# Performance work log

Measured on AMD Instinct MI355X. Metric: run time of the kernel, lower is better.

The kernel has to match this reference:

```python
import jax, jax.numpy as jnp
import numpy as np

B, N, D, H = 8, 2048, 1024, 1024

def setup_inputs() -> dict:
    key = jax.random.key(0)
    ks = jax.random.split(key, 7)
    s = 1.0 / np.sqrt(D)
    return {
        "x": jax.random.normal(ks[0], (B, N, D), dtype=jnp.float32),
        "Wq": jax.random.uniform(ks[1], (D, H), jnp.float32, -s, s),
        "bq": jax.random.uniform(ks[2], (H,), jnp.float32, -s, s),
        "Wk": jax.random.uniform(ks[3], (D, H), jnp.float32, -s, s),
        "bk": jax.random.uniform(ks[4], (H,), jnp.float32, -s, s),
        "Wv": jax.random.uniform(ks[5], (D, H), jnp.float32, -s, s),
        "bv": jax.random.uniform(ks[6], (H,), jnp.float32, -s, s),
    }

def reference(x, Wq, bq, Wk, bk, Wv, bv):
    # q, k, v: [B, N, H]
    q = jnp.einsum('bnd,dh->bnh', x, Wq) + bq
    k = jnp.einsum('bnd,dh->bnh', x, Wk) + bk
    v = jnp.einsum('bnd,dh->bnh', x, Wv) + bv
    scale = 1.0 / jnp.sqrt(jnp.asarray(q.shape[-1], q.dtype))
    score = jnp.einsum('bqh,bkh->bqk', q, k) * scale  # [B, N, N]
    causal = jnp.tril(jnp.ones((q.shape[1], q.shape[1]), dtype=bool))
    score = jnp.where(causal, score, -jnp.inf)
    attn = jax.nn.softmax(score, axis=-1)
    # dropout p=0.0 -> identity (deterministic reference)
    return jnp.einsum('bqk,bkh->bqh', attn, v)
```

## Files before the change

### kernel.cpp

```cpp
#include <hip/hip_runtime.h>
#include <hip/hip_bf16.h>
#include <stdint.h>

#define BB 8
#define NN 2048
#define DD 1024
#define HH 1024

using f32x4 = __attribute__((ext_vector_type(4))) float;
using s16x8 = __attribute__((ext_vector_type(8))) short;

__device__ __forceinline__ short f2bf(float f){
  union { float f; uint32_t u; } v; v.f = f;
  uint32_t r = (v.u + 0x7fffu + ((v.u >> 16) & 1u)) >> 16;
  return (short)r;
}
__device__ __forceinline__ float bf2f(short s){
  union { uint32_t u; float f; } v; v.u = ((uint32_t)(uint16_t)s) << 16; return v.f;
}

#define MFMA(a,b,c) __builtin_amdgcn_mfma_f32_16x16x32_bf16((a),(b),(c),0,0,0)

#define GL16(gp, lp) __builtin_amdgcn_global_load_lds( \
    (const __attribute__((address_space(1))) void*)(gp), \
    (__attribute__((address_space(3))) void*)(lp), 16, 0, 0)

__global__ __launch_bounds__(256) void k_conv_x(const float* __restrict__ x,
                                                short* __restrict__ xb){
  int gid = blockIdx.x*256 + threadIdx.x;
  const float4* xv = (const float4*)x;
  float4 a = xv[(size_t)gid*2], b2 = xv[(size_t)gid*2+1];
  s16x8 o;
  o[0]=f2bf(a.x);  o[1]=f2bf(a.y);  o[2]=f2bf(a.z);  o[3]=f2bf(a.w);
  o[4]=f2bf(b2.x); o[5]=f2bf(b2.y); o[6]=f2bf(b2.z); o[7]=f2bf(b2.w);
  *(s16x8*)(xb + (size_t)gid*8) = o;
}

__global__ __launch_bounds__(256) void k_conv_w(const float* __restrict__ Wq,
                                                const float* __restrict__ Wk,
                                                const float* __restrict__ Wv,
                                                short* __restrict__ Wt){
  __shared__ float tile[64][65];
  int bx = blockIdx.x; int mat = bx >> 8; int ti = bx & 255;
  int d0 = (ti >> 4) << 6, h0 = (ti & 15) << 6;
  const float* W = (mat==0) ? Wq : (mat==1 ? Wk : Wv);
  int t = threadIdx.x;
  for (int i=0;i<16;i++){ int e = i*256 + t; int r = e>>6, c = e&63;
    tile[r][c] = W[(size_t)(d0+r)*HH + h0 + c]; }
  __syncthreads();
  for (int i=0;i<16;i++){ int e = i*256 + t; int r = e>>6, c = e&63;
    Wt[(size_t)(mat*HH + h0 + r)*DD + d0 + c] = f2bf(tile[c][r]); }
}

__global__ __launch_bounds__(512,2) void k_gemm(const short* __restrict__ Aw,
                                                const short* __restrict__ Bw,
                                                const float* __restrict__ bq,
                                                const float* __restrict__ bk,
                                                const float* __restrict__ bv,
                                                short* __restrict__ Qw,
                                                short* __restrict__ Kw,
                                                short* __restrict__ Vt){
  __shared__ short Al[4][256*32];
  __shared__ short Bl[4][256*32];
  const int t = threadIdx.x, l = t & 63, w = t >> 6;
  const int g = l >> 4, c = l & 15;
  const int bid = blockIdx.x;
  const int bm = (bid & 7)*8 + ((bid >> 3) & 7);
  const int bn = bid >> 6;
  const int m0 = bm << 8, c0 = bn << 8;
  const int wr = w >> 2, wc = w & 3;
  f32x4 acc[8][4] = {};

  const int sr = t >> 2, sch = t & 3;
  const int u0 = sch ^ ((sr >> 1) & 3);
  const int u1 = sch ^ (((sr + 128) >> 1) & 3);
  const short* A0 = Aw + (size_t)(m0 + sr)*DD + u0*8;
  const short* A1 = Aw + (size_t)(m0 + sr + 128)*DD + u1*8;
  const short* B0 = Bw + (size_t)(c0 + sr)*DD + u0*8;
  const short* B1 = Bw + (size_t)(c0 + sr + 128)*DD + u1*8;
  const int d0b = sr*64 + sch*16, d1b = (sr+128)*64 + sch*16;
  auto stage = [&](int kt){
    int s = kt & 3, ko = kt*32;
    GL16(A0 + ko, (char*)&Al[s][0] + d0b);
    GL16(A1 + ko, (char*)&Al[s][0] + d1b);
    GL16(B0 + ko, (char*)&Bl[s][0] + d0b);
    GL16(B1 + ko, (char*)&Bl[s][0] + d1b);
  };

  int aoff[8], boff[4];
  #pragma unroll
  for (int mi=0;mi<8;mi++){
    int row = wr*128 + mi*16 + c;
    aoff[mi] = row*32 + (g ^ ((row>>1)&3))*8;
  }
  #pragma unroll
  for (int ni=0;ni<4;ni++){
    int row = wc*64 + ni*16 + c;
    boff[ni] = row*32 + (g ^ ((row>>1)&3))*8;
  }

  auto body = [&](int kt, bool dostage){
    int s = kt & 3;
    __builtin_amdgcn_sched_barrier(0);
    __builtin_amdgcn_s_barrier();
    __builtin_amdgcn_sched_barrier(0);
    s16x8 bfr[4], af[8];
    #pragma unroll
    for (int ni=0;ni<4;ni++) bfr[ni] = *(const s16x8*)&Bl[s][boff[ni]];
    #pragma unroll
    for (int mi=0;mi<8;mi++) af[mi] = *(const s16x8*)&Al[s][aoff[mi]];
    if (dostage) stage(kt+3);
    __builtin_amdgcn_s_setprio(1);
    #pragma unroll
    for (int mi=0;mi<8;mi++)
      #pragma unroll
      for (int ni=0;ni<4;ni++)
        acc[mi][ni] = MFMA(bfr[ni], af[mi], acc[mi][ni]);
    __builtin_amdgcn_s_setprio(0);
  };

  stage(0); stage(1); stage(2);
  for (int kt = 0; kt < 30; ++kt){
    asm volatile("s_waitcnt vmcnt(8)" ::: "memory");
    body(kt, kt < 29);
  }
  asm volatile("s_waitcnt vmcnt(4)" ::: "memory");
  body(30, false);
  asm volatile("s_waitcnt vmcnt(0)" ::: "memory");
  body(31, false);

  const int mat = bn >> 2;
  const float* bias = (mat==0) ? bq : (mat==1 ? bk : bv);
  if (mat < 2){
    short* Outp = (mat==0) ? Qw : Kw;
    #pragma unroll
    for (int ni=0;ni<4;ni++){
      int col0 = (bn & 3)*256 + wc*64 + ni*16 + g*4;
      float4 bv4 = *(const float4*)&bias[col0];
      #pragma unroll
      for (int mi=0;mi<8;mi++){
        int orow = m0 + wr*128 + mi*16 + c;
        short4 pk;
        pk.x = f2bf(acc[mi][ni][0] + bv4.x);
        pk.y = f2bf(acc[mi][ni][1] + bv4.y);
        pk.z = f2bf(acc[mi][ni][2] + bv4.z);
        pk.w = f2bf(acc[mi][ni][3] + bv4.w);
        *(short4*)&Outp[(size_t)orow*HH + col0] = pk;
      }
    }
  } else {
    short* S = (w < 4) ? ((short*)&Al[0][0] + w*4352)
                       : ((short*)&Bl[0][0] + (w-4)*4352);
    const int bb = m0 >> 11;
    const int nbase = m0 & 2047;
    const int hglob0 = (bn & 3)*256 + wc*64;
    #pragma unroll
    for (int rr = 0; rr < 2; ++rr){
      const int R = 2*wr + rr;
      asm volatile("" ::: "memory");
      #pragma unroll
      for (int ni=0;ni<4;ni++){
        int col0 = hglob0 + ni*16 + g*4;
        float4 bv4 = *(const float4*)&bias[col0];
        #pragma unroll
        for (int mi2=0;mi2<4;mi2++){
          short4 pk;
          pk.x = f2bf(acc[rr*4+mi2][ni][0] + bv4.x);
          pk.y = f2bf(acc[rr*4+mi2][ni][1] + bv4.y);
          pk.z = f2bf(acc[rr*4+mi2][ni][2] + bv4.z);
          pk.w = f2bf(acc[rr*4+mi2][ni][3] + bv4.w);
          *(short4*)&S[(mi2*16 + c)*68 + ni*16 + g*4] = pk;
        }
      }
      asm volatile("" ::: "memory");
      #pragma unroll
      for (int k=0;k<8;++k){
        int hr = (l>>3) + k*8;
        int ng = l & 7;
        s16x8 sv;
        #pragma unroll
        for (int e=0;e<8;e++) sv[e] = S[(ng*8+e)*68 + hr];
        *(s16x8*)&Vt[((size_t)bb*HH + hglob0 + hr)*NN + nbase + R*64 + ng*8] = sv;
      }
    }
  }
}

__global__ __launch_bounds__(512) void k_s(const short* __restrict__ Qw,
                                           const short* __restrict__ Kw,
                                           short* __restrict__ Pp){
  __shared__ short Ql[128*32];
  __shared__ short Kl[256*32];
  const int t = threadIdx.x, l = t & 63, w = t >> 6;
  const int g = l >> 4, c = l & 15;
  int p = blockIdx.x; int b = p & 7; int si = p >> 3;
  int tr = 0; while ((((tr+2)*(tr+2)) >> 2) <= si) tr++;
  int tcp = si - (((tr+1)*(tr+1)) >> 2);
  const float SC_EXP = 0.04508422002783268f;
  const int wq = w >> 2, wk = w & 3;
  f32x4 acc[4][4] = {};

  const int sr = t >> 2, sch = t & 3;
  const int su  = sch ^ ((sr >> 1) & 3);
  const int su2 = sch ^ (((sr + 128) >> 1) & 3);
  const short* Qs  = Qw + ((size_t)(b*NN + tr*128  + sr))*HH + su*8;
  const short* Ks0 = Kw + ((size_t)(b*NN + tcp*256 + sr))*HH + su*8;
  const short* Ks1 = Kw + ((size_t)(b*NN + tcp*256 + sr + 128))*HH + su2*8;

  const int rchunk = (g ^ ((c>>1)&3)) * 8;
  int qoff[4], koff[4];
  #pragma unroll
  for (int mi=0;mi<4;mi++) qoff[mi] = (wq*64 + mi*16 + c)*32 + rchunk;
  #pragma unroll
  for (int ni=0;ni<4;ni++) koff[ni] = (wk*64 + ni*16 + c)*32 + rchunk;

  for (int kt = 0; kt < 32; ++kt){
    int ko = kt*32;
    __syncthreads();
    GL16(Qs  + ko, (char*)Ql + t*16);
    GL16(Ks0 + ko, (char*)Kl + t*16);
    GL16(Ks1 + ko, (char*)Kl + 8192 + t*16);
    __syncthreads();
    s16x8 qf[4], kf[4];
    #pragma unroll
    for (int ni=0;ni<4;ni++) kf[ni] = *(const s16x8*)&Kl[koff[ni]];
    #pragma unroll
    for (int mi=0;mi<4;mi++) qf[mi] = *(const s16x8*)&Ql[qoff[mi]];
    #pragma unroll
    for (int mi=0;mi<4;mi++)
      #pragma unroll
      for (int ni=0;ni<4;ni++)
        acc[mi][ni] = MFMA(kf[ni], qf[mi], acc[mi][ni]);
  }

  short* Pt = Pp + ((size_t)(b*72 + si))*32768;
  #pragma unroll
  for (int ni=0;ni<4;ni++){
    int pc0 = wk*64 + ni*16 + g*4;
    #pragma unroll
    for (int mi=0;mi<4;mi++){
      int pr = wq*64 + mi*16 + c;
      short4 pk;
      #pragma unroll
      for (int i=0;i<4;i++){
        bool keep = (tcp*256 + pc0 + i) <= (tr*128 + pr);
        float pv = keep ? exp2f(acc[mi][ni][i]*SC_EXP) : 0.f;
        ((short*)&pk)[i] = f2bf(pv);
      }
      *(short4*)&Pt[pr*256 + pc0] = pk;
    }
  }
}

__global__ __launch_bounds__(512) void k_pv(const short* __restrict__ Pp,
                                            const short* __restrict__ Vt,
                                            float* __restrict__ out){
  __shared__ short Pl[128*32];
  __shared__ short Vl[256*32];
  const int t = threadIdx.x, l = t & 63, w = t >> 6;
  const int g = l >> 4, c = l & 15;
  int p = blockIdx.x;
  int r = p >> 8, j = p & 255;
  int tr = r ? (15 - (j >> 4)) : (j >> 4);
  int id = r ? (16 + (j & 15)) : (j & 15);
  int b = id & 7, hc = id >> 3;
  const short* Pb = Pp + ((size_t)(b*72 + (((tr+1)*(tr+1))>>2)))*32768;
  const int wq = w >> 2, wh = w & 3;
  f32x4 acc[4][4] = {};
  float ls[4] = {0.f,0.f,0.f,0.f};

  const int sr = t >> 2, sch = t & 3;
  const int su  = sch ^ ((sr >> 1) & 3);
  const int su2 = sch ^ (((sr + 128) >> 1) & 3);
  const short* Vs0 = Vt + ((size_t)(b*HH + hc*256 + sr))*NN + su*8;
  const short* Vs1 = Vt + ((size_t)(b*HH + hc*256 + sr + 128))*NN + su2*8;

  const int rchunk = (g ^ ((c>>1)&3)) * 8;
  int poff[4], voff[4];
  #pragma unroll
  for (int mi=0;mi<4;mi++) poff[mi] = (wq*64 + mi*16 + c)*32 + rchunk;
  #pragma unroll
  for (int ni=0;ni<4;ni++) voff[ni] = (wh*64 + ni*16 + c)*32 + rchunk;

  const int nst = ((tr + 2) >> 1) * 8;
  for (int kt = 0; kt < nst; ++kt){
    const short* Ps = Pb + (size_t)(kt>>3)*32768 + (kt&7)*32;
    __syncthreads();
    GL16(Ps + sr*256 + su*8, (char*)Pl + t*16);
    GL16(Vs0 + kt*32, (char*)Vl + t*16);
    GL16(Vs1 + kt*32, (char*)Vl + 8192 + t*16);
    __syncthreads();
    s16x8 pf[4], vf[4];
    #pragma unroll
    for (int ni=0;ni<4;ni++) vf[ni] = *(const s16x8*)&Vl[voff[ni]];
    #pragma unroll
    for (int mi=0;mi<4;mi++) pf[mi] = *(const s16x8*)&Pl[poff[mi]];
    #pragma unroll
    for (int mi=0;mi<4;mi++){
      #pragma unroll
      for (int e=0;e<8;e++) ls[mi] += bf2f(pf[mi][e]);
    }
    #pragma unroll
    for (int mi=0;mi<4;mi++)
      #pragma unroll
      for (int ni=0;ni<4;ni++)
        acc[mi][ni] = MFMA(vf[ni], pf[mi], acc[mi][ni]);
  }
  #pragma unroll
  for (int mi=0;mi<4;mi++){
    ls[mi] += __shfl_xor(ls[mi], 16);
    ls[mi] += __shfl_xor(ls[mi], 32);
  }
  #pragma unroll
  for (int mi=0;mi<4;mi++){
    float linv = 1.0f / ls[mi];
    int orow = tr*128 + wq*64 + mi*16 + c;
    #pragma unroll
    for (int ni=0;ni<4;ni++){
      int h0 = hc*256 + wh*64 + ni*16 + g*4;
      float4 o4;
      o4.x = acc[mi][ni][0]*linv; o4.y = acc[mi][ni][1]*linv;
      o4.z = acc[mi][ni][2]*linv; o4.w = acc[mi][ni][3]*linv;
      *(float4*)&out[((size_t)(b*NN + orow))*HH + h0] = o4;
    }
  }
}

extern "C" void kernel_launch(void* const* d_in, const int* in_sizes, int n_in,
                              void* d_out, int out_size, void* d_ws, size_t ws_size,
                              hipStream_t stream) {
  const float* x  = (const float*)d_in[0];
  const float* Wq = (const float*)d_in[1];
  const float* bq = (const float*)d_in[2];
  const float* Wk = (const float*)d_in[3];
  const float* bk = (const float*)d_in[4];
  const float* Wv = (const float*)d_in[5];
  const float* bv = (const float*)d_in[6];
  char* ws = (char*)d_ws;
  short* xb = (short*)(ws);
  short* Pp = (short*)(ws);
  short* Wt = (short*)(ws + 33554432u);
  short* Qw = (short*)(ws + 41943040u);
  short* Kw = (short*)(ws + 75497472u);
  short* Vt = (short*)(ws + 109051904u);

  k_conv_x<<<8192, 256, 0, stream>>>(x, xb);
  k_conv_w<<<768, 256, 0, stream>>>(Wq, Wk, Wv, Wt);
  k_gemm<<<768, 512, 0, stream>>>(xb, Wt, bq, bk, bv, Qw, Kw, Vt);
  k_s<<<576, 512, 0, stream>>>(Qw, Kw, Pp);
  k_pv<<<512, 512, 0, stream>>>(Pp, Vt, (float*)d_out);
}
```

Measured before the change: 281.4 us.

## Load GEMM B operand directly to registers, drop B shared-memory staging

In the QKV projection GEMM, the B (weight) tiles no longer go through LDS. Each wave loads its B fragments straight from global memory into registers, double-buffered one k-step ahead, while A keeps its 4-stage LDS pipeline. This halves LDS usage, which could allow higher occupancy, and removes the LDS reads for B. The cost is redundant global loads of B across the two wave rows, more registers, and an extra sync plus an unpadded transpose scratch layout in the V epilogue that may cause bank conflicts.

New measurement: 330.7 us. +17.5%, slower.

```diff
diff --git a/kernel.cpp b/kernel.cpp
--- a/kernel.cpp
+++ b/kernel.cpp
@@ -61,7 +61,6 @@
                                                 short* __restrict__ Kw,
                                                 short* __restrict__ Vt){
   __shared__ short Al[4][256*32];
-  __shared__ short Bl[4][256*32];
   const int t = threadIdx.x, l = t & 63, w = t >> 6;
   const int g = l >> 4, c = l & 15;
   const int bid = blockIdx.x;
@@ -76,58 +75,61 @@
   const int u1 = sch ^ (((sr + 128) >> 1) & 3);
   const short* A0 = Aw + (size_t)(m0 + sr)*DD + u0*8;
   const short* A1 = Aw + (size_t)(m0 + sr + 128)*DD + u1*8;
-  const short* B0 = Bw + (size_t)(c0 + sr)*DD + u0*8;
-  const short* B1 = Bw + (size_t)(c0 + sr + 128)*DD + u1*8;
   const int d0b = sr*64 + sch*16, d1b = (sr+128)*64 + sch*16;
-  auto stage = [&](int kt){
+  auto stageA = [&](int kt){
     int s = kt & 3, ko = kt*32;
     GL16(A0 + ko, (char*)&Al[s][0] + d0b);
     GL16(A1 + ko, (char*)&Al[s][0] + d1b);
-    GL16(B0 + ko, (char*)&Bl[s][0] + d0b);
-    GL16(B1 + ko, (char*)&Bl[s][0] + d1b);
   };
 
-  int aoff[8], boff[4];
+  int aoff[8];
   #pragma unroll
   for (int mi=0;mi<8;mi++){
     int row = wr*128 + mi*16 + c;
     aoff[mi] = row*32 + (g ^ ((row>>1)&3))*8;
   }
-  #pragma unroll
-  for (int ni=0;ni<4;ni++){
-    int row = wc*64 + ni*16 + c;
-    boff[ni] = row*32 + (g ^ ((row>>1)&3))*8;
-  }
-
-  auto body = [&](int kt, bool dostage){
-    int s = kt & 3;
+  const short* Bp[4];
+  #pragma unroll
+  for (int ni=0;ni<4;ni++)
+    Bp[ni] = Bw + (size_t)(c0 + wc*64 + ni*16 + c)*DD + g*8;
+
+  s16x8 bfrE[4], bfrO[4];
+
+  auto body = [&](int kt, s16x8 (&cur)[4], s16x8 (&nxt)[4]){
+    if (kt == 0)      { asm volatile("s_waitcnt vmcnt(4)" ::: "memory"); }
+    else if (kt < 30) { asm volatile("s_waitcnt vmcnt(2)" ::: "memory"); }
+    else              { asm volatile("s_waitcnt vmcnt(0)" ::: "memory"); }
     __builtin_amdgcn_sched_barrier(0);
     __builtin_amdgcn_s_barrier();
     __builtin_amdgcn_sched_barrier(0);
-    s16x8 bfr[4], af[8];
-    #pragma unroll
-    for (int ni=0;ni<4;ni++) bfr[ni] = *(const s16x8*)&Bl[s][boff[ni]];
+    const int s = kt & 3;
+    s16x8 af[8];
     #pragma unroll
     for (int mi=0;mi<8;mi++) af[mi] = *(const s16x8*)&Al[s][aoff[mi]];
-    if (dostage) stage(kt+3);
+    if (kt < 31){
+      const int ko = (kt+1)*32;
+      #pragma unroll
+      for (int ni=0;ni<4;ni++) nxt[ni] = *(const s16x8*)(Bp[ni] + ko);
+    }
+    if (kt < 29) stageA(kt+3);
+    __builtin_amdgcn_sched_barrier(0);
     __builtin_amdgcn_s_setprio(1);
     #pragma unroll
     for (int mi=0;mi<8;mi++)
       #pragma unroll
       for (int ni=0;ni<4;ni++)
-        acc[mi][ni] = MFMA(bfr[ni], af[mi], acc[mi][ni]);
+        acc[mi][ni] = MFMA(cur[ni], af[mi], acc[mi][ni]);
     __builtin_amdgcn_s_setprio(0);
   };
 
-  stage(0); stage(1); stage(2);
-  for (int kt = 0; kt < 30; ++kt){
-    asm volatile("s_waitcnt vmcnt(8)" ::: "memory");
-    body(kt, kt < 29);
-  }
-  asm volatile("s_waitcnt vmcnt(4)" ::: "memory");
-  body(30, false);
-  asm volatile("s_waitcnt vmcnt(0)" ::: "memory");
-  body(31, false);
+  #pragma unroll
+  for (int ni=0;ni<4;ni++) bfrE[ni] = *(const s16x8*)(Bp[ni]);
+  stageA(0); stageA(1); stageA(2);
+
+  for (int k2 = 0; k2 < 16; ++k2){
+    body(2*k2,     bfrE, bfrO);
+    body(2*k2 + 1, bfrO, bfrE);
+  }
 
   const int mat = bn >> 2;
   const float* bias = (mat==0) ? bq : (mat==1 ? bk : bv);
@@ -149,8 +151,8 @@
       }
     }
   } else {
-    short* S = (w < 4) ? ((short*)&Al[0][0] + w*4352)
-                       : ((short*)&Bl[0][0] + (w-4)*4352);
+    __syncthreads();
+    short* S = (short*)&Al[0][0] + w*4096;
     const int bb = m0 >> 11;
     const int nbase = m0 & 2047;
     const int hglob0 = (bn & 3)*256 + wc*64;
@@ -169,7 +171,7 @@
           pk.y = f2bf(acc[rr*4+mi2][ni][1] + bv4.y);
           pk.z = f2bf(acc[rr*4+mi2][ni][2] + bv4.z);
           pk.w = f2bf(acc[rr*4+mi2][ni][3] + bv4.w);
-          *(short4*)&S[(mi2*16 + c)*68 + ni*16 + g*4] = pk;
+          *(short4*)&S[(mi2*16 + c)*64 + ni*16 + g*4] = pk;
         }
       }
       asm volatile("" ::: "memory");
@@ -179,9 +181,11 @@
         int ng = l & 7;
         s16x8 sv;
         #pragma unroll
-        for (int e=0;e<8;e++) sv[e] = S[(ng*8+e)*68 + hr];
+        for (int e=0;e<8;e++) sv[e] = S[(ng*8+e)*64 + hr];
         *(s16x8*)&Vt[((size_t)bb*HH + hglob0 + hr)*NN + nbase + R*64 + ng*8] = sv;
       }
+      asm volatile("" ::: "memory");
+      __syncthreads();
     }
   }
 }
```
